# Performance work log

Hardware: AMD Instinct MI355X
Metric: run time of the kernel (lower is better)

The kernel has to match this reference:

```python
import jax, jax.numpy as jnp
import numpy as np

EMB = 384
HEAD_DIM = 64  # emb_size / num_head = 384 / 6
B, S = 8, 2048


def setup_inputs() -> dict:
    key = jax.random.key(0)
    k1, k2, k3, k4 = jax.random.split(key, 4)
    x = jax.random.normal(k1, (B, S, EMB), dtype=jnp.float32)
    # nn.Linear(emb, head_dim, bias=False): store as [in, out] so q = x @ W
    scale = 0.02
    Wq = jax.random.normal(k2, (EMB, HEAD_DIM), dtype=jnp.float32) * scale
    Wk = jax.random.normal(k3, (EMB, HEAD_DIM), dtype=jnp.float32) * scale
    Wv = jax.random.normal(k4, (EMB, HEAD_DIM), dtype=jnp.float32) * scale
    return {"x": x, "Wq": Wq, "Wk": Wk, "Wv": Wv}


def reference(x, Wq, Wk, Wv):
    # x: [B, S, C]
    q = jnp.einsum('bsc,cd->bsd', x, Wq)  # [B,S,D]
    k = jnp.einsum('bsc,cd->bsd', x, Wk)
    v = jnp.einsum('bsc,cd->bsd', x, Wv)
    scores = jnp.einsum('bid,bjd->bij', q, k) * (HEAD_DIM ** -0.5)  # [B,S,S]
    # causal mask: positions with tril==0 (j > i) set to -inf
    causal = jnp.tril(jnp.ones((S, S), dtype=bool))  # [S,S]
    scores = jnp.where(causal[None, :, :], scores, -jnp.inf)
    # NOTE: faithful to original — softmax over dim=1 (query axis), not -1.
    attn = jax.nn.softmax(scores, axis=1)  # [B,S,S]
    out = jnp.einsum('bij,bjd->bid', attn, v)  # [B,S,D]
    return out
```

## Files before the change

kernel.cpp:

```cpp
#include <hip/hip_runtime.h>
#include <hip/hip_bf16.h>
#include <math.h>

#define B_N 8
#define S_N 2048
#define C_N 384
#define D_N 64
#define NPART 4
#define NEG_BIG (-1e30f)

typedef __bf16 bf16x8 __attribute__((ext_vector_type(8)));
typedef float f32x4 __attribute__((ext_vector_type(4)));

static __device__ __forceinline__ bf16x8 ldfrag(const __bf16* p) {
  return *reinterpret_cast<const bf16x8*>(p);
}

static __device__ __forceinline__ void gload16(void* lds, const void* gsrc) {
  __builtin_amdgcn_global_load_lds(
      (const __attribute__((address_space(1))) unsigned int*)gsrc,
      (__attribute__((address_space(3))) unsigned int*)lds, 16, 0, 0);
}

__global__ __launch_bounds__(256) void prep(
    const float* __restrict__ x,
    const float* __restrict__ Wq, const float* __restrict__ Wk,
    const float* __restrict__ Wv,
    __bf16* __restrict__ xb, __bf16* __restrict__ Wt) {
  const int blk = blockIdx.x;
  if (blk < 36) {
    const int idx = blk * 2048 + threadIdx.x * 8;
    const int m = idx / (64 * C_N);
    const int r = idx % (64 * C_N);
    const int d = r / C_N;
    const int c = r % C_N;
    const float* W = (m == 0) ? Wq : (m == 1) ? Wk : Wv;
    const float s = (m == 0) ? 0.125f : 1.0f;
    bf16x8 v;
#pragma unroll
    for (int i = 0; i < 8; ++i) v[i] = (__bf16)(W[(c + i) * 64 + d] * s);
    *reinterpret_cast<bf16x8*>(Wt + idx) = v;
  } else {
    const size_t idx = (size_t)(blk - 36) * 2048 + (size_t)threadIdx.x * 8;
    const float4 a = *reinterpret_cast<const float4*>(x + idx);
    const float4 b = *reinterpret_cast<const float4*>(x + idx + 4);
    bf16x8 v;
    v[0] = (__bf16)a.x; v[1] = (__bf16)a.y; v[2] = (__bf16)a.z; v[3] = (__bf16)a.w;
    v[4] = (__bf16)b.x; v[5] = (__bf16)b.y; v[6] = (__bf16)b.z; v[7] = (__bf16)b.w;
    *reinterpret_cast<bf16x8*>(xb + idx) = v;
  }
}

__global__ __launch_bounds__(384) void qkv_mfma(
    const __bf16* __restrict__ xb, const __bf16* __restrict__ Wt,
    __bf16* __restrict__ Q, __bf16* __restrict__ K, __bf16* __restrict__ Vt) {
  const int t = threadIdx.x;
  const int w = t >> 6, lane = t & 63, lr = lane & 15, lg = lane >> 4;
  const int mat = w >> 1, nh = w & 1;
  const int row0 = blockIdx.x * 16;

  __shared__ __bf16 vtile[16][68];

  const __bf16* xr = xb + (size_t)(row0 + lr) * C_N;
  const __bf16* Wm = Wt + (size_t)mat * 64 * C_N;

  f32x4 acc0 = {0.f, 0.f, 0.f, 0.f};
  f32x4 acc1 = {0.f, 0.f, 0.f, 0.f};

  bf16x8 a   = ldfrag(xr + lg * 8);
  bf16x8 bw0 = ldfrag(Wm + (size_t)(nh * 32 + lr) * C_N + lg * 8);
  bf16x8 bw1 = ldfrag(Wm + (size_t)(nh * 32 + 16 + lr) * C_N + lg * 8);

  for (int kk = 0; kk < C_N / 32; ++kk) {
    const int kn = (kk + 1 < C_N / 32) ? kk + 1 : kk;
    const bf16x8 an   = ldfrag(xr + kn * 32 + lg * 8);
    const bf16x8 b0n  = ldfrag(Wm + (size_t)(nh * 32 + lr) * C_N + kn * 32 + lg * 8);
    const bf16x8 b1n  = ldfrag(Wm + (size_t)(nh * 32 + 16 + lr) * C_N + kn * 32 + lg * 8);

    acc0 = __builtin_amdgcn_mfma_f32_16x16x32_bf16(a, bw0, acc0, 0, 0, 0);
    acc1 = __builtin_amdgcn_mfma_f32_16x16x32_bf16(a, bw1, acc1, 0, 0, 0);

    a = an; bw0 = b0n; bw1 = b1n;
  }

  if (mat < 2) {
    __bf16* outp = (mat == 0) ? Q : K;
#pragma unroll
    for (int r = 0; r < 4; ++r) {
      outp[(size_t)(row0 + lg * 4 + r) * 64 + nh * 32 + lr] = (__bf16)acc0[r];
      outp[(size_t)(row0 + lg * 4 + r) * 64 + nh * 32 + 16 + lr] = (__bf16)acc1[r];
    }
  } else {
#pragma unroll
    for (int r = 0; r < 4; ++r) {
      vtile[lg * 4 + r][nh * 32 + lr] = (__bf16)acc0[r];
      vtile[lg * 4 + r][nh * 32 + 16 + lr] = (__bf16)acc1[r];
    }
  }
  __syncthreads();

  const int b = row0 >> 11, s0 = row0 & (S_N - 1);
  for (int idx = t; idx < 64 * 16; idx += 384) {
    const int d = idx >> 4, s2 = idx & 15;
    Vt[((size_t)b * D_N + d) * S_N + s0 + s2] = vtile[s2][d];
  }
}

__global__ __launch_bounds__(512) void col_stats(
    const __bf16* __restrict__ Q, const __bf16* __restrict__ K,
    float* __restrict__ zpart) {
  const int wg = blockIdx.x;
  const int b  = wg & 7;
  const int jb = (wg >> 3) & 15;
  const int h  = wg >> 7;
  const int j0 = jb * 128;

  const int t = threadIdx.x;
  const int q = t >> 6;
  const int lane = t & 63, lr = lane & 15, lg = lane >> 4;

  const int n = 32 - 2 * jb;
  const int itStart = 2 * jb + (n * h) / NPART;
  const int itEnd   = 2 * jb + (n * (h + 1)) / NPART;
  float* zout = zpart + (size_t)h * B_N * S_N + (size_t)b * S_N;

  if (itStart >= itEnd) {
    if (lg == 0) zout[j0 + q * 16 + lr] = 0.f;
    return;
  }

  __shared__ __align__(16) __bf16 QT[2][64][64];

  const __bf16* Qb = Q + (size_t)b * S_N * 64;
  const __bf16* Kb = K + (size_t)b * S_N * 64;

  const int jg = j0 + q * 16 + lr;
  const bf16x8 bk0 = ldfrag(Kb + (size_t)jg * 64 + lg * 8);
  const bf16x8 bk1 = ldfrag(Kb + (size_t)jg * 64 + 32 + lg * 8);

  const int r0 = t >> 3, c0 = t & 7;
  const int gq = c0 ^ (r0 & 7);

#define STAGE_Q(BUF, TILE) \
  gload16(&QT[BUF][r0][c0 * 8], Qb + (size_t)((TILE) * 64 + r0) * 64 + gq * 8)

  STAGE_Q(0, itStart);
  __syncthreads();

  float z = 0.f;
  int cur = 0;
  for (int it = itStart; it < itEnd; ++it) {
    const int i0 = it * 64;
    if (it + 1 < itEnd) STAGE_Q(cur ^ 1, it + 1);

#pragma unroll
    for (int s = 0; s < 4; ++s) {
      const int arow = s * 16 + lr;
      const bf16x8 aq0 = ldfrag(&QT[cur][arow][(lg ^ (arow & 7)) * 8]);
      const bf16x8 aq1 = ldfrag(&QT[cur][arow][((4 + lg) ^ (arow & 7)) * 8]);
      f32x4 s4 = {0.f, 0.f, 0.f, 0.f};
      s4 = __builtin_amdgcn_mfma_f32_16x16x32_bf16(aq0, bk0, s4, 0, 0, 0);
      s4 = __builtin_amdgcn_mfma_f32_16x16x32_bf16(aq1, bk1, s4, 0, 0, 0);
      const int ibase = i0 + s * 16 + lg * 4;
      float es = 0.f;
#pragma unroll
      for (int r = 0; r < 4; ++r)
        es += (ibase + r >= jg) ? __expf(s4[r]) : 0.f;
      es += __shfl_xor(es, 16);
      es += __shfl_xor(es, 32);
      z += es;
    }

    __syncthreads();
    cur ^= 1;
  }
#undef STAGE_Q

  if (lg == 0) zout[jg] = z;
}

__global__ __launch_bounds__(512) void attn_out(
    const __bf16* __restrict__ Q, const __bf16* __restrict__ K,
    const __bf16* __restrict__ Vt, const float* __restrict__ zpart,
    float* __restrict__ opart) {
  const int wg = blockIdx.x;
  const int b  = wg & 7;
  const int ib = (wg >> 3) & 15;
  const int h  = wg >> 7;

  const int t = threadIdx.x;
  const int s = t >> 6;
  const int lane = t & 63, lr = lane & 15, lg = lane >> 4;
  const int i0 = ib * 128;

  const int n = 2 * ib + 2;
  const int jbStart = (n * h) / NPART;
  const int jbEnd   = (n * (h + 1)) / NPART;

  float* op = opart + (size_t)h * B_N * S_N * D_N + (size_t)b * S_N * D_N;
  const int ibase = i0 + s * 16 + lg * 4;

  f32x4 o[4];
#pragma unroll
  for (int dt = 0; dt < 4; ++dt) o[dt] = {0.f, 0.f, 0.f, 0.f};

  if (jbStart < jbEnd) {
    __shared__ __align__(16) __bf16 KT[2][64][64];
    __shared__ __align__(16) __bf16 VT[2][64][64];
    __shared__ __align__(16) __bf16 P[8][16][72];

    const __bf16* Qb  = Q  + (size_t)b * S_N * 64;
    const __bf16* Kb  = K  + (size_t)b * S_N * 64;
    const __bf16* Vtb = Vt + (size_t)b * D_N * S_N;
    const float*  zp  = zpart + (size_t)b * S_N;

    const int r0 = t >> 3, c0 = t & 7;
    const int gq = c0 ^ (r0 & 7);

#define STAGE_KV(BUF, TJ0) do { \
      gload16(&KT[BUF][r0][c0 * 8], Kb + (size_t)((TJ0) + r0) * 64 + gq * 8); \
      gload16(&VT[BUF][r0][c0 * 8], Vtb + (size_t)r0 * S_N + (TJ0) + gq * 8); \
    } while (0)

    const int ri = i0 + s * 16 + lr;
    const bf16x8 aq0 = ldfrag(Qb + (size_t)ri * 64 + lg * 8);
    const bf16x8 aq1 = ldfrag(Qb + (size_t)ri * 64 + 32 + lg * 8);

    STAGE_KV(0, jbStart * 64);
    __syncthreads();

    int cur = 0;
    for (int jb = jbStart; jb < jbEnd; ++jb) {
      const int j0 = jb * 64;
      if (jb + 1 < jbEnd) STAGE_KV(cur ^ 1, j0 + 64);

#pragma unroll
      for (int jt = 0; jt < 4; ++jt) {
        const int krow = jt * 16 + lr;
        const bf16x8 bk0 = ldfrag(&KT[cur][krow][(lg ^ (krow & 7)) * 8]);
        const bf16x8 bk1 = ldfrag(&KT[cur][krow][((4 + lg) ^ (krow & 7)) * 8]);
        f32x4 s4 = {0.f, 0.f, 0.f, 0.f};
        s4 = __builtin_amdgcn_mfma_f32_16x16x32_bf16(aq0, bk0, s4, 0, 0, 0);
        s4 = __builtin_amdgcn_mfma_f32_16x16x32_bf16(aq1, bk1, s4, 0, 0, 0);
        const int jg = j0 + jt * 16 + lr;
        const float rz = 1.0f / (zp[jg] + zp[(size_t)B_N * S_N + jg] +
                                 zp[(size_t)2 * B_N * S_N + jg] +
                                 zp[(size_t)3 * B_N * S_N + jg]);
#pragma unroll
        for (int r = 0; r < 4; ++r) {
          const float pv = (jg <= ibase + r) ? __expf(s4[r]) * rz : 0.f;
          P[s][lg * 4 + r][jt * 16 + lr] = (__bf16)pv;
        }
      }

      const bf16x8 ap0 = ldfrag(&P[s][lr][lg * 8]);
      const bf16x8 ap1 = ldfrag(&P[s][lr][32 + lg * 8]);
#pragma unroll
      for (int dt = 0; dt < 4; ++dt) {
        const int vrow = dt * 16 + lr;
        const bf16x8 bv0 = ldfrag(&VT[cur][vrow][(lg ^ (vrow & 7)) * 8]);
        const bf16x8 bv1 = ldfrag(&VT[cur][vrow][((4 + lg) ^ (vrow & 7)) * 8]);
        o[dt] = __builtin_amdgcn_mfma_f32_16x16x32_bf16(ap0, bv0, o[dt], 0, 0, 0);
        o[dt] = __builtin_amdgcn_mfma_f32_16x16x32_bf16(ap1, bv1, o[dt], 0, 0, 0);
      }

      __syncthreads();
      cur ^= 1;
    }
#undef STAGE_KV
  }

#pragma unroll
  for (int dt = 0; dt < 4; ++dt)
#pragma unroll
    for (int r = 0; r < 4; ++r)
      op[(size_t)(ibase + r) * D_N + dt * 16 + lr] = o[dt][r];
}

__global__ __launch_bounds__(256) void combine(
    const float* __restrict__ opart, float* __restrict__ out) {
  const size_t idx = (size_t)blockIdx.x * 256 + threadIdx.x;
  const size_t stride = (size_t)B_N * S_N * D_N;
  out[idx] = opart[idx] + opart[stride + idx] + opart[2 * stride + idx] +
             opart[3 * stride + idx];
}

extern "C" void kernel_launch(void* const* d_in, const int* in_sizes, int n_in,
                              void* d_out, int out_size, void* d_ws, size_t ws_size,
                              hipStream_t stream) {
  (void)in_sizes; (void)n_in; (void)ws_size; (void)out_size;
  const float* x  = (const float*)d_in[0];
  const float* Wq = (const float*)d_in[1];
  const float* Wk = (const float*)d_in[2];
  const float* Wv = (const float*)d_in[3];
  float* out = (float*)d_out;

  __bf16* Qb = (__bf16*)d_ws;
  __bf16* Kb = Qb + (size_t)B_N * S_N * D_N;
  __bf16* Vt = Kb + (size_t)B_N * S_N * D_N;
  float* zpart = (float*)(Vt + (size_t)B_N * S_N * D_N);
  float* opart = zpart + (size_t)NPART * B_N * S_N;
  __bf16* Wt = (__bf16*)(opart + (size_t)NPART * B_N * S_N * D_N);
  __bf16* xbuf = Wt + (size_t)3 * 64 * C_N;

  prep<<<dim3(36 + B_N * S_N * C_N / 2048), dim3(256), 0, stream>>>(
      x, Wq, Wk, Wv, xbuf, Wt);
  qkv_mfma<<<dim3(B_N * S_N / 16), dim3(384), 0, stream>>>(xbuf, Wt, Qb, Kb, Vt);
  col_stats<<<dim3(NPART * 16 * B_N), dim3(512), 0, stream>>>(Qb, Kb, zpart);
  attn_out<<<dim3(NPART * 16 * B_N), dim3(512), 0, stream>>>(Qb, Kb, Vt, zpart, opart);
  combine<<<dim3(B_N * S_N * D_N / 256), dim3(256), 0, stream>>>(opart, out);
}
```

Before: 77.63 us.

## Fuse all stages into one cooperative persistent kernel with grid syncs

Merges the prep, QKV projection, column-stats, attention-output and combine kernels into a single cooperative kernel of 256 blocks that separates the phases with grid.sync(). The split factor over the causal range drops from 4 to 2, so the partial sums and combine pass shrink and the whole work fits in one wave of 256 workgroups. The aim is to remove multiple launch gaps and tail effects. In exchange, grid barriers add their own cost, per-block work becomes uneven with the causal split, and the conversion and projection phases now run on fewer threads.

```diff
diff --git a/kernel.cpp b/kernel.cpp
--- a/kernel.cpp
+++ b/kernel.cpp
@@ -1,13 +1,15 @@
 #include <hip/hip_runtime.h>
 #include <hip/hip_bf16.h>
+#include <hip/hip_cooperative_groups.h>
 #include <math.h>
+
+namespace cg = cooperative_groups;
 
 #define B_N 8
 #define S_N 2048
 #define C_N 384
 #define D_N 64
-#define NPART 4
-#define NEG_BIG (-1e30f)
+#define NPART 2
 
 typedef __bf16 bf16x8 __attribute__((ext_vector_type(8)));
 typedef float f32x4 __attribute__((ext_vector_type(4)));
@@ -22,195 +24,183 @@
       (__attribute__((address_space(3))) unsigned int*)lds, 16, 0, 0);
 }
 
-__global__ __launch_bounds__(256) void prep(
+__global__ __launch_bounds__(512) void fused(
     const float* __restrict__ x,
     const float* __restrict__ Wq, const float* __restrict__ Wk,
     const float* __restrict__ Wv,
-    __bf16* __restrict__ xb, __bf16* __restrict__ Wt) {
+    __bf16* __restrict__ xb, __bf16* __restrict__ Wt,
+    __bf16* __restrict__ Qb, __bf16* __restrict__ Kb, __bf16* __restrict__ Vt,
+    float* __restrict__ zpart, float* __restrict__ opart,
+    float* __restrict__ out) {
+  cg::grid_group grid = cg::this_grid();
+
+  __shared__ __align__(16) unsigned char smem[51200];
+
   const int blk = blockIdx.x;
-  if (blk < 36) {
-    const int idx = blk * 2048 + threadIdx.x * 8;
-    const int m = idx / (64 * C_N);
-    const int r = idx % (64 * C_N);
-    const int d = r / C_N;
-    const int c = r % C_N;
-    const float* W = (m == 0) ? Wq : (m == 1) ? Wk : Wv;
-    const float s = (m == 0) ? 0.125f : 1.0f;
-    bf16x8 v;
-#pragma unroll
-    for (int i = 0; i < 8; ++i) v[i] = (__bf16)(W[(c + i) * 64 + d] * s);
-    *reinterpret_cast<bf16x8*>(Wt + idx) = v;
-  } else {
-    const size_t idx = (size_t)(blk - 36) * 2048 + (size_t)threadIdx.x * 8;
-    const float4 a = *reinterpret_cast<const float4*>(x + idx);
-    const float4 b = *reinterpret_cast<const float4*>(x + idx + 4);
-    bf16x8 v;
-    v[0] = (__bf16)a.x; v[1] = (__bf16)a.y; v[2] = (__bf16)a.z; v[3] = (__bf16)a.w;
-    v[4] = (__bf16)b.x; v[5] = (__bf16)b.y; v[6] = (__bf16)b.z; v[7] = (__bf16)b.w;
-    *reinterpret_cast<bf16x8*>(xb + idx) = v;
-  }
-}
-
-__global__ __launch_bounds__(384) void qkv_mfma(
-    const __bf16* __restrict__ xb, const __bf16* __restrict__ Wt,
-    __bf16* __restrict__ Q, __bf16* __restrict__ K, __bf16* __restrict__ Vt) {
   const int t = threadIdx.x;
-  const int w = t >> 6, lane = t & 63, lr = lane & 15, lg = lane >> 4;
-  const int mat = w >> 1, nh = w & 1;
-  const int row0 = blockIdx.x * 16;
-
-  __shared__ __bf16 vtile[16][68];
-
-  const __bf16* xr = xb + (size_t)(row0 + lr) * C_N;
-  const __bf16* Wm = Wt + (size_t)mat * 64 * C_N;
-
-  f32x4 acc0 = {0.f, 0.f, 0.f, 0.f};
-  f32x4 acc1 = {0.f, 0.f, 0.f, 0.f};
-
-  bf16x8 a   = ldfrag(xr + lg * 8);
-  bf16x8 bw0 = ldfrag(Wm + (size_t)(nh * 32 + lr) * C_N + lg * 8);
-  bf16x8 bw1 = ldfrag(Wm + (size_t)(nh * 32 + 16 + lr) * C_N + lg * 8);
-
-  for (int kk = 0; kk < C_N / 32; ++kk) {
-    const int kn = (kk + 1 < C_N / 32) ? kk + 1 : kk;
-    const bf16x8 an   = ldfrag(xr + kn * 32 + lg * 8);
-    const bf16x8 b0n  = ldfrag(Wm + (size_t)(nh * 32 + lr) * C_N + kn * 32 + lg * 8);
-    const bf16x8 b1n  = ldfrag(Wm + (size_t)(nh * 32 + 16 + lr) * C_N + kn * 32 + lg * 8);
-
-    acc0 = __builtin_amdgcn_mfma_f32_16x16x32_bf16(a, bw0, acc0, 0, 0, 0);
-    acc1 = __builtin_amdgcn_mfma_f32_16x16x32_bf16(a, bw1, acc1, 0, 0, 0);
-
-    a = an; bw0 = b0n; bw1 = b1n;
-  }
-
-  if (mat < 2) {
-    __bf16* outp = (mat == 0) ? Q : K;
-#pragma unroll
-    for (int r = 0; r < 4; ++r) {
-      outp[(size_t)(row0 + lg * 4 + r) * 64 + nh * 32 + lr] = (__bf16)acc0[r];
-      outp[(size_t)(row0 + lg * 4 + r) * 64 + nh * 32 + 16 + lr] = (__bf16)acc1[r];
-    }
-  } else {
-#pragma unroll
-    for (int r = 0; r < 4; ++r) {
-      vtile[lg * 4 + r][nh * 32 + lr] = (__bf16)acc0[r];
-      vtile[lg * 4 + r][nh * 32 + 16 + lr] = (__bf16)acc1[r];
-    }
-  }
-  __syncthreads();
-
-  const int b = row0 >> 11, s0 = row0 & (S_N - 1);
-  for (int idx = t; idx < 64 * 16; idx += 384) {
-    const int d = idx >> 4, s2 = idx & 15;
-    Vt[((size_t)b * D_N + d) * S_N + s0 + s2] = vtile[s2][d];
-  }
-}
-
-__global__ __launch_bounds__(512) void col_stats(
-    const __bf16* __restrict__ Q, const __bf16* __restrict__ K,
-    float* __restrict__ zpart) {
-  const int wg = blockIdx.x;
-  const int b  = wg & 7;
-  const int jb = (wg >> 3) & 15;
-  const int h  = wg >> 7;
-  const int j0 = jb * 128;
-
-  const int t = threadIdx.x;
-  const int q = t >> 6;
   const int lane = t & 63, lr = lane & 15, lg = lane >> 4;
 
-  const int n = 32 - 2 * jb;
-  const int itStart = 2 * jb + (n * h) / NPART;
-  const int itEnd   = 2 * jb + (n * (h + 1)) / NPART;
-  float* zout = zpart + (size_t)h * B_N * S_N + (size_t)b * S_N;
-
-  if (itStart >= itEnd) {
-    if (lg == 0) zout[j0 + q * 16 + lr] = 0.f;
-    return;
-  }
-
-  __shared__ __align__(16) __bf16 QT[2][64][64];
-
-  const __bf16* Qb = Q + (size_t)b * S_N * 64;
-  const __bf16* Kb = K + (size_t)b * S_N * 64;
-
-  const int jg = j0 + q * 16 + lr;
-  const bf16x8 bk0 = ldfrag(Kb + (size_t)jg * 64 + lg * 8);
-  const bf16x8 bk1 = ldfrag(Kb + (size_t)jg * 64 + 32 + lg * 8);
-
-  const int r0 = t >> 3, c0 = t & 7;
-  const int gq = c0 ^ (r0 & 7);
+  {
+    const int gtid = blk * 512 + t;
+    const int gsz = 256 * 512;
+    for (int ch = gtid; ch < 9216; ch += gsz) {
+      const int idx = ch * 8;
+      const int m = idx / (64 * C_N);
+      const int r = idx % (64 * C_N);
+      const int d = r / C_N;
+      const int c = r % C_N;
+      const float* W = (m == 0) ? Wq : (m == 1) ? Wk : Wv;
+      const float s = (m == 0) ? 0.125f : 1.0f;
+      bf16x8 v;
+#pragma unroll
+      for (int i = 0; i < 8; ++i) v[i] = (__bf16)(W[(c + i) * 64 + d] * s);
+      *reinterpret_cast<bf16x8*>(Wt + idx) = v;
+    }
+    for (size_t ch = gtid; ch < (size_t)B_N * S_N * C_N / 8; ch += gsz) {
+      const size_t idx = ch * 8;
+      const float4 a = *reinterpret_cast<const float4*>(x + idx);
+      const float4 b = *reinterpret_cast<const float4*>(x + idx + 4);
+      bf16x8 v;
+      v[0] = (__bf16)a.x; v[1] = (__bf16)a.y; v[2] = (__bf16)a.z; v[3] = (__bf16)a.w;
+      v[4] = (__bf16)b.x; v[5] = (__bf16)b.y; v[6] = (__bf16)b.z; v[7] = (__bf16)b.w;
+      *reinterpret_cast<bf16x8*>(xb + idx) = v;
+    }
+  }
+  grid.sync();
+
+  {
+    __bf16 (*vtile)[68] = reinterpret_cast<__bf16(*)[68]>(smem);
+    const int w = t >> 6;
+    const int mat = w >> 1, nh = w & 1;
+#pragma unroll
+    for (int r16 = 0; r16 < 4; ++r16) {
+      const int row0 = blk * 64 + r16 * 16;
+      if (w < 6) {
+        const __bf16* xr = xb + (size_t)(row0 + lr) * C_N;
+        const __bf16* Wm = Wt + (size_t)mat * 64 * C_N;
+        f32x4 acc0 = {0.f, 0.f, 0.f, 0.f};
+        f32x4 acc1 = {0.f, 0.f, 0.f, 0.f};
+        bf16x8 a   = ldfrag(xr + lg * 8);
+        bf16x8 bw0 = ldfrag(Wm + (size_t)(nh * 32 + lr) * C_N + lg * 8);
+        bf16x8 bw1 = ldfrag(Wm + (size_t)(nh * 32 + 16 + lr) * C_N + lg * 8);
+        for (int kk = 0; kk < C_N / 32; ++kk) {
+          const int kn = (kk + 1 < C_N / 32) ? kk + 1 : kk;
+          const bf16x8 an  = ldfrag(xr + kn * 32 + lg * 8);
+          const bf16x8 b0n = ldfrag(Wm + (size_t)(nh * 32 + lr) * C_N + kn * 32 + lg * 8);
+          const bf16x8 b1n = ldfrag(Wm + (size_t)(nh * 32 + 16 + lr) * C_N + kn * 32 + lg * 8);
+          acc0 = __builtin_amdgcn_mfma_f32_16x16x32_bf16(a, bw0, acc0, 0, 0, 0);
+          acc1 = __builtin_amdgcn_mfma_f32_16x16x32_bf16(a, bw1, acc1, 0, 0, 0);
+          a = an; bw0 = b0n; bw1 = b1n;
+        }
+        if (mat < 2) {
+          __bf16* outp = (mat == 0) ? Qb : Kb;
+#pragma unroll
+          for (int r = 0; r < 4; ++r) {
+            outp[(size_t)(row0 + lg * 4 + r) * 64 + nh * 32 + lr] = (__bf16)acc0[r];
+            outp[(size_t)(row0 + lg * 4 + r) * 64 + nh * 32 + 16 + lr] = (__bf16)acc1[r];
+          }
+        } else {
+#pragma unroll
+          for (int r = 0; r < 4; ++r) {
+            vtile[lg * 4 + r][nh * 32 + lr] = (__bf16)acc0[r];
+            vtile[lg * 4 + r][nh * 32 + 16 + lr] = (__bf16)acc1[r];
+          }
+        }
+      }
+      __syncthreads();
+      const int b = row0 >> 11, s0 = row0 & (S_N - 1);
+      for (int idx = t; idx < 64 * 16; idx += 512) {
+        const int d = idx >> 4, s2 = idx & 15;
+        Vt[((size_t)b * D_N + d) * S_N + s0 + s2] = vtile[s2][d];
+      }
+      __syncthreads();
+    }
+  }
+  grid.sync();
+
+  {
+    __bf16 (*QT)[64][64] = reinterpret_cast<__bf16(*)[64][64]>(smem);
+    const int b  = blk & 7;
+    const int jb = (blk >> 3) & 15;
+    const int h  = blk >> 7;
+    const int j0 = jb * 128;
+    const int q = t >> 6;
+
+    const int n = 32 - 2 * jb;
+    const int itStart = 2 * jb + (n * h) / NPART;
+    const int itEnd   = 2 * jb + (n * (h + 1)) / NPART;
+    float* zout = zpart + (size_t)h * B_N * S_N + (size_t)b * S_N;
+
+    const __bf16* Qp = Qb + (size_t)b * S_N * 64;
+    const __bf16* Kp = Kb + (size_t)b * S_N * 64;
+
+    const int jg = j0 + q * 16 + lr;
+    const bf16x8 bk0 = ldfrag(Kp + (size_t)jg * 64 + lg * 8);
+    const bf16x8 bk1 = ldfrag(Kp + (size_t)jg * 64 + 32 + lg * 8);
+
+    const int r0 = t >> 3, c0 = t & 7;
+    const int gq = c0 ^ (r0 & 7);
 
 #define STAGE_Q(BUF, TILE) \
-  gload16(&QT[BUF][r0][c0 * 8], Qb + (size_t)((TILE) * 64 + r0) * 64 + gq * 8)
-
-  STAGE_Q(0, itStart);
-  __syncthreads();
-
-  float z = 0.f;
-  int cur = 0;
-  for (int it = itStart; it < itEnd; ++it) {
-    const int i0 = it * 64;
-    if (it + 1 < itEnd) STAGE_Q(cur ^ 1, it + 1);
-
-#pragma unroll
-    for (int s = 0; s < 4; ++s) {
-      const int arow = s * 16 + lr;
-      const bf16x8 aq0 = ldfrag(&QT[cur][arow][(lg ^ (arow & 7)) * 8]);
-      const bf16x8 aq1 = ldfrag(&QT[cur][arow][((4 + lg) ^ (arow & 7)) * 8]);
-      f32x4 s4 = {0.f, 0.f, 0.f, 0.f};
-      s4 = __builtin_amdgcn_mfma_f32_16x16x32_bf16(aq0, bk0, s4, 0, 0, 0);
-      s4 = __builtin_amdgcn_mfma_f32_16x16x32_bf16(aq1, bk1, s4, 0, 0, 0);
-      const int ibase = i0 + s * 16 + lg * 4;
-      float es = 0.f;
-#pragma unroll
-      for (int r = 0; r < 4; ++r)
-        es += (ibase + r >= jg) ? __expf(s4[r]) : 0.f;
-      es += __shfl_xor(es, 16);
-      es += __shfl_xor(es, 32);
-      z += es;
-    }
-
+    gload16(&QT[BUF][r0][c0 * 8], Qp + (size_t)((TILE) * 64 + r0) * 64 + gq * 8)
+
+    STAGE_Q(0, itStart);
     __syncthreads();
-    cur ^= 1;
-  }
+
+    float z = 0.f;
+    int cur = 0;
+    for (int it = itStart; it < itEnd; ++it) {
+      const int i0 = it * 64;
+      if (it + 1 < itEnd) STAGE_Q(cur ^ 1, it + 1);
+#pragma unroll
+      for (int s = 0; s < 4; ++s) {
+        const int arow = s * 16 + lr;
+        const bf16x8 aq0 = ldfrag(&QT[cur][arow][(lg ^ (arow & 7)) * 8]);
+        const bf16x8 aq1 = ldfrag(&QT[cur][arow][((4 + lg) ^ (arow & 7)) * 8]);
+        f32x4 s4 = {0.f, 0.f, 0.f, 0.f};
+        s4 = __builtin_amdgcn_mfma_f32_16x16x32_bf16(aq0, bk0, s4, 0, 0, 0);
+        s4 = __builtin_amdgcn_mfma_f32_16x16x32_bf16(aq1, bk1, s4, 0, 0, 0);
+        const int ibase = i0 + s * 16 + lg * 4;
+        float es = 0.f;
+#pragma unroll
+        for (int r = 0; r < 4; ++r)
+          es += (ibase + r >= jg) ? __expf(s4[r]) : 0.f;
+        es += __shfl_xor(es, 16);
+        es += __shfl_xor(es, 32);
+        z += es;
+      }
+      __syncthreads();
+      cur ^= 1;
+    }
 #undef STAGE_Q
-
-  if (lg == 0) zout[jg] = z;
-}
-
-__global__ __launch_bounds__(512) void attn_out(
-    const __bf16* __restrict__ Q, const __bf16* __restrict__ K,
-    const __bf16* __restrict__ Vt, const float* __restrict__ zpart,
-    float* __restrict__ opart) {
-  const int wg = blockIdx.x;
-  const int b  = wg & 7;
-  const int ib = (wg >> 3) & 15;
-  const int h  = wg >> 7;
-
-  const int t = threadIdx.x;
-  const int s = t >> 6;
-  const int lane = t & 63, lr = lane & 15, lg = lane >> 4;
-  const int i0 = ib * 128;
-
-  const int n = 2 * ib + 2;
-  const int jbStart = (n * h) / NPART;
-  const int jbEnd   = (n * (h + 1)) / NPART;
-
-  float* op = opart + (size_t)h * B_N * S_N * D_N + (size_t)b * S_N * D_N;
-  const int ibase = i0 + s * 16 + lg * 4;
-
-  f32x4 o[4];
-#pragma unroll
-  for (int dt = 0; dt < 4; ++dt) o[dt] = {0.f, 0.f, 0.f, 0.f};
-
-  if (jbStart < jbEnd) {
-    __shared__ __align__(16) __bf16 KT[2][64][64];
-    __shared__ __align__(16) __bf16 VT[2][64][64];
-    __shared__ __align__(16) __bf16 P[8][16][72];
-
-    const __bf16* Qb  = Q  + (size_t)b * S_N * 64;
-    const __bf16* Kb  = K  + (size_t)b * S_N * 64;
+    if (lg == 0) zout[jg] = z;
+  }
+  grid.sync();
+
+  {
+    __bf16 (*KT)[64][64] = reinterpret_cast<__bf16(*)[64][64]>(smem);
+    __bf16 (*VT)[64][64] = reinterpret_cast<__bf16(*)[64][64]>(smem + 16384);
+    __bf16 (*P)[16][72]  = reinterpret_cast<__bf16(*)[16][72]>(smem + 32768);
+
+    const int b  = blk & 7;
+    const int ib = (blk >> 3) & 15;
+    const int h  = blk >> 7;
+    const int s = t >> 6;
+    const int i0 = ib * 128;
+
+    const int n = 2 * ib + 2;
+    const int jbStart = (n * h) / NPART;
+    const int jbEnd   = (n * (h + 1)) / NPART;
+
+    float* op = opart + (size_t)h * B_N * S_N * D_N + (size_t)b * S_N * D_N;
+    const int ibase = i0 + s * 16 + lg * 4;
+
+    f32x4 o[4];
+#pragma unroll
+    for (int dt = 0; dt < 4; ++dt) o[dt] = {0.f, 0.f, 0.f, 0.f};
+
+    const __bf16* Qp  = Qb + (size_t)b * S_N * 64;
+    const __bf16* Kp  = Kb + (size_t)b * S_N * 64;
     const __bf16* Vtb = Vt + (size_t)b * D_N * S_N;
     const float*  zp  = zpart + (size_t)b * S_N;
 
@@ -218,13 +208,13 @@
     const int gq = c0 ^ (r0 & 7);
 
 #define STAGE_KV(BUF, TJ0) do { \
-      gload16(&KT[BUF][r0][c0 * 8], Kb + (size_t)((TJ0) + r0) * 64 + gq * 8); \
+      gload16(&KT[BUF][r0][c0 * 8], Kp + (size_t)((TJ0) + r0) * 64 + gq * 8); \
       gload16(&VT[BUF][r0][c0 * 8], Vtb + (size_t)r0 * S_N + (TJ0) + gq * 8); \
     } while (0)
 
     const int ri = i0 + s * 16 + lr;
-    const bf16x8 aq0 = ldfrag(Qb + (size_t)ri * 64 + lg * 8);
-    const bf16x8 aq1 = ldfrag(Qb + (size_t)ri * 64 + 32 + lg * 8);
+    const bf16x8 aq0 = ldfrag(Qp + (size_t)ri * 64 + lg * 8);
+    const bf16x8 aq1 = ldfrag(Qp + (size_t)ri * 64 + 32 + lg * 8);
 
     STAGE_KV(0, jbStart * 64);
     __syncthreads();
@@ -233,7 +223,6 @@
     for (int jb = jbStart; jb < jbEnd; ++jb) {
       const int j0 = jb * 64;
       if (jb + 1 < jbEnd) STAGE_KV(cur ^ 1, j0 + 64);
-
 #pragma unroll
       for (int jt = 0; jt < 4; ++jt) {
         const int krow = jt * 16 + lr;
@@ -243,16 +232,13 @@
         s4 = __builtin_amdgcn_mfma_f32_16x16x32_bf16(aq0, bk0, s4, 0, 0, 0);
         s4 = __builtin_amdgcn_mfma_f32_16x16x32_bf16(aq1, bk1, s4, 0, 0, 0);
         const int jg = j0 + jt * 16 + lr;
-        const float rz = 1.0f / (zp[jg] + zp[(size_t)B_N * S_N + jg] +
-                                 zp[(size_t)2 * B_N * S_N + jg] +
-                                 zp[(size_t)3 * B_N * S_N + jg]);
+        const float rz = 1.0f / (zp[jg] + zp[(size_t)B_N * S_N + jg]);
 #pragma unroll
         for (int r = 0; r < 4; ++r) {
           const float pv = (jg <= ibase + r) ? __expf(s4[r]) * rz : 0.f;
           P[s][lg * 4 + r][jt * 16 + lr] = (__bf16)pv;
         }
       }
-
       const bf16x8 ap0 = ldfrag(&P[s][lr][lg * 8]);
       const bf16x8 ap1 = ldfrag(&P[s][lr][32 + lg * 8]);
 #pragma unroll
@@ -263,26 +249,30 @@
         o[dt] = __builtin_amdgcn_mfma_f32_16x16x32_bf16(ap0, bv0, o[dt], 0, 0, 0);
         o[dt] = __builtin_amdgcn_mfma_f32_16x16x32_bf16(ap1, bv1, o[dt], 0, 0, 0);
       }
-
       __syncthreads();
       cur ^= 1;
     }
 #undef STAGE_KV
-  }
-
-#pragma unroll
-  for (int dt = 0; dt < 4; ++dt)
-#pragma unroll
-    for (int r = 0; r < 4; ++r)
-      op[(size_t)(ibase + r) * D_N + dt * 16 + lr] = o[dt][r];
-}
-
-__global__ __launch_bounds__(256) void combine(
-    const float* __restrict__ opart, float* __restrict__ out) {
-  const size_t idx = (size_t)blockIdx.x * 256 + threadIdx.x;
-  const size_t stride = (size_t)B_N * S_N * D_N;
-  out[idx] = opart[idx] + opart[stride + idx] + opart[2 * stride + idx] +
-             opart[3 * stride + idx];
+
+#pragma unroll
+    for (int dt = 0; dt < 4; ++dt)
+#pragma unroll
+      for (int r = 0; r < 4; ++r)
+        op[(size_t)(ibase + r) * D_N + dt * 16 + lr] = o[dt][r];
+  }
+  grid.sync();
+
+  {
+    const size_t stride = (size_t)B_N * S_N * D_N;
+    const int gtid = blk * 512 + t;
+    for (size_t idx4 = gtid; idx4 < stride / 4; idx4 += 256 * 512) {
+      const float4 a = *reinterpret_cast<const float4*>(opart + idx4 * 4);
+      const float4 b = *reinterpret_cast<const float4*>(opart + stride + idx4 * 4);
+      float4 r;
+      r.x = a.x + b.x; r.y = a.y + b.y; r.z = a.z + b.z; r.w = a.w + b.w;
+      *reinterpret_cast<float4*>(out + idx4 * 4) = r;
+    }
+  }
 }
 
 extern "C" void kernel_launch(void* const* d_in, const int* in_sizes, int n_in,
@@ -303,10 +293,9 @@
   __bf16* Wt = (__bf16*)(opart + (size_t)NPART * B_N * S_N * D_N);
   __bf16* xbuf = Wt + (size_t)3 * 64 * C_N;
 
-  prep<<<dim3(36 + B_N * S_N * C_N / 2048), dim3(256), 0, stream>>>(
-      x, Wq, Wk, Wv, xbuf, Wt);
-  qkv_mfma<<<dim3(B_N * S_N / 16), dim3(384), 0, stream>>>(xbuf, Wt, Qb, Kb, Vt);
-  col_stats<<<dim3(NPART * 16 * B_N), dim3(512), 0, stream>>>(Qb, Kb, zpart);
-  attn_out<<<dim3(NPART * 16 * B_N), dim3(512), 0, stream>>>(Qb, Kb, Vt, zpart, opart);
-  combine<<<dim3(B_N * S_N * D_N / 256), dim3(256), 0, stream>>>(opart, out);
+  void* args[] = {(void*)&x, (void*)&Wq, (void*)&Wk, (void*)&Wv,
+                  (void*)&xbuf, (void*)&Wt, (void*)&Qb, (void*)&Kb, (void*)&Vt,
+                  (void*)&zpart, (void*)&opart, (void*)&out};
+  hipLaunchCooperativeKernel((const void*)fused, dim3(256), dim3(512), args, 0,
+                             stream);
 }
```

Result: slower. 204.2 us (+163.0%).
